# Optimization experiments

Measured on AMD Instinct MI355X. Metric: run time of the kernel, lower is better.

## Reference

```python
import jax, jax.numpy as jnp
import numpy as np

B, T, D = 2, 2048, 1024
HEADS, UNITS = 16, 64
OUT_DIM = 1024
_LARGE_BIAS = 10000.0


def _uniform(key, shape, fan_in, fan_out):
    limit = np.sqrt(6.0 / (fan_in + fan_out))
    return jax.random.uniform(key, shape, jnp.float32, -limit, limit)


def setup_inputs() -> dict:
    key = jax.random.key(0)
    kx, kq, kk, kv, ko = jax.random.split(key, 5)
    x = jax.random.normal(kx, (B, T, D), jnp.float32)
    mask = jnp.ones((B, T), jnp.int32)
    Wq = _uniform(kq, (D, HEADS * UNITS), D, UNITS)
    Wk = _uniform(kk, (D, HEADS * UNITS), D, UNITS)
    Wv = _uniform(kv, (D, HEADS * UNITS), D, UNITS)
    Wo = _uniform(ko, (HEADS * UNITS, OUT_DIM), HEADS * UNITS, OUT_DIM)
    return {"x": x, "mask": mask, "Wq": Wq, "Wk": Wk, "Wv": Wv, "Wo": Wo}


def reference(x, mask, Wq, Wk, Wv, Wo):
    m = mask.astype(x.dtype)                      # [B, T]
    x = x * m[:, :, None]                         # zero padded positions
    b, t, _ = x.shape
    # projections, split heads: [B, T, H, U]
    q = (x @ Wq).reshape(b, t, HEADS, UNITS)
    k = (x @ Wk).reshape(b, t, HEADS, UNITS)
    v = (x @ Wv).reshape(b, t, HEADS, UNITS)
    # logits[b,h,i,j] = sum_u q[b,i,h,u] k[b,j,h,u]
    logits = jnp.einsum('bihu,bjhu->bhij', q, k) / np.sqrt(UNITS).astype(x.dtype)
    # causal (forward) mask: subtract large bias above the diagonal
    causal = jnp.triu(jnp.full((t, t), _LARGE_BIAS, x.dtype), k=1)
    logits = logits - causal
    # padding mask on key axis
    logits = logits - ((1.0 - m) * _LARGE_BIAS)[:, None, None, :]
    weights = jax.nn.softmax(logits, axis=-1)     # [B, H, T, T]
    attended = jnp.einsum('bhij,bjhu->bihu', weights, v)
    attended = attended.reshape(b, t, HEADS * UNITS)
    return attended @ Wo                          # [B, T, OUT_DIM]
```

## Files before the change

kernel.cpp:

```cpp
#include <hip/hip_runtime.h>
#include <stdint.h>
#include <stddef.h>

#define B_ 2
#define T_ 2048
#define D_ 1024
#define H_ 16
#define U_ 64
#define M_ (B_ * T_)
#define N_ (H_ * U_)

typedef __attribute__((ext_vector_type(4))) float f32x4;
typedef __attribute__((ext_vector_type(8))) short s16x8;
typedef __attribute__((ext_vector_type(8))) __bf16 b16x8;

static_assert(sizeof(s16x8) == 16, "frag size");

__device__ __forceinline__ unsigned short f2bf(float f) {
  unsigned int u = __float_as_uint(f);
  u += 0x7FFFu + ((u >> 16) & 1u);
  return (unsigned short)(u >> 16);
}

__device__ __forceinline__ float exp2_hw(float x) {
  float r;
  asm("v_exp_f32 %0, %1" : "=v"(r) : "v"(x));
  return r;
}
__device__ __forceinline__ unsigned int cvtpk_bf16(float lo, float hi) {
  unsigned int r;
  asm("v_cvt_pk_bf16_f32 %0, %1, %2" : "=v"(r) : "v"(lo), "v"(hi));
  return r;
}

template <typename V>
__device__ __forceinline__ auto mfma16_impl(V a, V b, f32x4 c, int)
    -> decltype(__builtin_amdgcn_mfma_f32_16x16x32_bf16(a, b, c, 0, 0, 0)) {
  return __builtin_amdgcn_mfma_f32_16x16x32_bf16(a, b, c, 0, 0, 0);
}
template <typename V>
__device__ __forceinline__ f32x4 mfma16_impl(V a, V b, f32x4 c, long) {
  return __builtin_amdgcn_mfma_f32_16x16x32_bf16(
      __builtin_bit_cast(b16x8, a), __builtin_bit_cast(b16x8, b), c, 0, 0, 0);
}
__device__ __forceinline__ f32x4 mfma16(s16x8 a, s16x8 b, f32x4 c) {
  return mfma16_impl(a, b, c, 0);
}

__device__ __forceinline__ void gld16(const unsigned short* g, unsigned short* l) {
  __builtin_amdgcn_global_load_lds(
      (const __attribute__((address_space(1))) void*)g,
      (__attribute__((address_space(3))) void*)l, 16, 0, 0);
}

__global__ void wtrans_kernel(const float* __restrict__ w0, const float* __restrict__ w1,
                              const float* __restrict__ w2, const float* __restrict__ w3,
                              unsigned short* __restrict__ o0, unsigned short* __restrict__ o1,
                              unsigned short* __restrict__ o2, unsigned short* __restrict__ o3) {
  __shared__ float tile[64][65];
  const float* w;
  unsigned short* o;
  switch (blockIdx.z) {
    case 0: w = w0; o = o0; break;
    case 1: w = w1; o = o1; break;
    case 2: w = w2; o = o2; break;
    default: w = w3; o = o3; break;
  }
  const int kb = blockIdx.y * 64, nb = blockIdx.x * 64;
  const int tid = threadIdx.x;
  const int r0 = tid >> 6, c = tid & 63;
#pragma unroll
  for (int i = 0; i < 16; i++) {
    int r = i * 4 + r0;
    tile[r][c] = w[(size_t)(kb + r) * 1024 + nb + c];
  }
  __syncthreads();
#pragma unroll
  for (int i = 0; i < 16; i++) {
    int r = i * 4 + r0;
    o[(size_t)(nb + r) * 1024 + kb + c] = f2bf(tile[c][r]);
  }
}

__global__ void xmask_kernel(const float* __restrict__ x, const int* __restrict__ mask,
                             unsigned short* __restrict__ xb) {
  const int idx = (blockIdx.x * 256 + threadIdx.x) * 4;
  const int row = idx >> 10;
  const float m = (float)mask[row];
  float4 v = *(const float4*)(x + idx);
  ushort4 o;
  o.x = f2bf(v.x * m);
  o.y = f2bf(v.y * m);
  o.z = f2bf(v.z * m);
  o.w = f2bf(v.w * m);
  *(ushort4*)(xb + idx) = o;
}

template <int MODE>
__device__ __forceinline__ void gemm97_body(const unsigned short* __restrict__ A,
                                            const unsigned short* __restrict__ Bt,
                                            void* __restrict__ Cout) {
  constexpr int Kd = 1024, Nd = 1024;
  __shared__ unsigned short la[128 * 32];
  __shared__ unsigned short lb[128 * 32];
  const int tid = threadIdx.x;
  const int lane = tid & 63;
  const int w = tid >> 6;
  const int mb = blockIdx.y * 128, nb = blockIdx.x * 128;
  const int wm = (w >> 1) * 64, wn = (w & 1) * 64;
  const int lr = lane & 15, lg = lane >> 4;
  const int srow = w * 16 + (lane >> 2);
  const int scol = (lane & 3) * 8;
  const unsigned short* gA = A + (size_t)(mb + srow) * Kd + scol;
  const unsigned short* gB = Bt + (size_t)(nb + srow) * Kd + scol;
  unsigned short* lA = la + srow * 32 + scol;
  unsigned short* lB = lb + srow * 32 + scol;

  f32x4 acc[4][4] = {};

  for (int kt = 0; kt < Kd; kt += 32) {
    gld16(gA + kt, lA);
    gld16(gA + kt + (size_t)64 * Kd, lA + 64 * 32);
    gld16(gB + kt, lB);
    gld16(gB + kt + (size_t)64 * Kd, lB + 64 * 32);
    __syncthreads();
    s16x8 af[4], bfr[4];
#pragma unroll
    for (int i = 0; i < 4; i++)
      af[i] = *(const s16x8*)(la + (wm + i * 16 + lr) * 32 + lg * 8);
#pragma unroll
    for (int j = 0; j < 4; j++)
      bfr[j] = *(const s16x8*)(lb + (wn + j * 16 + lr) * 32 + lg * 8);
#pragma unroll
    for (int i = 0; i < 4; i++)
#pragma unroll
      for (int j = 0; j < 4; j++)
        acc[i][j] = mfma16(af[i], bfr[j], acc[i][j]);
    __syncthreads();
  }

#pragma unroll
  for (int i = 0; i < 4; i++)
#pragma unroll
    for (int j = 0; j < 4; j++) {
      const int col = nb + wn + j * 16 + lr;
      const int rowb = mb + wm + i * 16 + lg * 4;
      if (MODE == 1) {
        float* C = (float*)Cout;
#pragma unroll
        for (int r = 0; r < 4; r++) C[(size_t)(rowb + r) * Nd + col] = acc[i][j][r];
      } else if (MODE == 0) {
        unsigned short* C = (unsigned short*)Cout;
#pragma unroll
        for (int r = 0; r < 4; r++) C[(size_t)(rowb + r) * Nd + col] = f2bf(acc[i][j][r]);
      } else {
        unsigned short* C = (unsigned short*)Cout;
        const size_t vrow = ((size_t)(rowb >> 11) * 16 + (col >> 6)) * 64 + (col & 63);
        ushort4 o;
#pragma unroll
        for (int r = 0; r < 4; r++) ((unsigned short*)&o)[r] = f2bf(acc[i][j][r]);
        *(ushort4*)(C + vrow * T_ + (rowb & 2047)) = o;
      }
    }
}

__global__ __launch_bounds__(256) void gemm_qkv(const unsigned short* __restrict__ A,
                                                const unsigned short* __restrict__ wq,
                                                const unsigned short* __restrict__ wk,
                                                const unsigned short* __restrict__ wv,
                                                unsigned short* __restrict__ cq,
                                                unsigned short* __restrict__ ck,
                                                unsigned short* __restrict__ vt) {
  if (blockIdx.z == 0) {
    gemm97_body<0>(A, wq, cq);
  } else if (blockIdx.z == 1) {
    gemm97_body<0>(A, wk, ck);
  } else {
    gemm97_body<2>(A, wv, vt);
  }
}

__global__ __launch_bounds__(256) void gemm_out(const unsigned short* __restrict__ A,
                                                const unsigned short* __restrict__ woT,
                                                float* __restrict__ C) {
  gemm97_body<1>(A, woT, C);
}

__global__ __launch_bounds__(64) void attn17_kernel(const unsigned short* __restrict__ Q,
                                                    const unsigned short* __restrict__ K,
                                                    const unsigned short* __restrict__ Vt,
                                                    const int* __restrict__ mask,
                                                    unsigned short* __restrict__ att) {
  __shared__ unsigned short pbuf[32 * 64];
  const int lane = threadIdx.x & 63;
  const int li = lane & 15, lg = lane >> 4;
  const int bh = blockIdx.x & 31;
  const int b = bh >> 4, h = bh & 15;
  const int pr = blockIdx.x >> 5;

  const float CS = 0.125f * 1.44269504089f;
  const float PB = 10000.0f * 1.44269504089f;
  const float THR = 8.0f;

  const unsigned short* Kb = K + (size_t)(b * T_) * 1024 + h * 64;
  const unsigned short* Vtb = Vt + (size_t)bh * 64 * T_;
  const int* mk = mask + b * T_;

  const int xr = (li & 3) << 5;
  char* pbb = (char*)pbuf;

  for (int g = 0; g < 2; g++) {
    const int qg = g == 0 ? (63 - pr) : pr;
    const int q0 = qg * 32;

    s16x8 qf[2][2];
#pragma unroll
    for (int f = 0; f < 2; f++) {
      const unsigned short* qrow = Q + ((size_t)(b * T_) + q0 + f * 16 + li) * 1024 + h * 64;
      qf[f][0] = *(const s16x8*)(qrow + lg * 8);
      qf[f][1] = *(const s16x8*)(qrow + 32 + lg * 8);
    }

    const int iq0 = q0 + li, iq1 = q0 + 16 + li;

    float mrun[2] = {-1e30f, -1e30f};
    f32x4 lp[2] = {};
    f32x4 acc[4][2] = {};
    s16x8 vf[4][2];

    const int ntiles = (q0 + 95) >> 6;

    auto loadK = [&](s16x8 (&dst)[4][2], int jb) {
#pragma unroll
      for (int jf = 0; jf < 4; jf++) {
        const unsigned short* kr = Kb + (size_t)(jb + jf * 16 + li) * 1024 + lg * 8;
        dst[jf][0] = *(const s16x8*)kr;
        dst[jf][1] = *(const s16x8*)(kr + 32);
      }
    };
    auto loadM = [&](int4 (&dst)[4], int jb) {
#pragma unroll
      for (int jf = 0; jf < 4; jf++)
        dst[jf] = *(const int4*)(mk + jb + jf * 16 + lg * 4);
    };
    auto loadV = [&](int jb) {
#pragma unroll
      for (int uf = 0; uf < 4; uf++) {
        const unsigned short* vr = Vtb + (size_t)(uf * 16 + li) * T_ + jb + lg * 8;
        vf[uf][0] = *(const s16x8*)vr;
        vf[uf][1] = *(const s16x8*)(vr + 32);
      }
    };
    auto qk = [&](f32x4 (&s)[4][2], s16x8 (&kc)[4][2]) {
      __builtin_amdgcn_s_setprio(1);
#pragma unroll
      for (int jf = 0; jf < 4; jf++) {
        f32x4 z = {};
        s[jf][0] = mfma16(kc[jf][0], qf[0][0], z);
        s[jf][0] = mfma16(kc[jf][1], qf[0][1], s[jf][0]);
        f32x4 z2 = {};
        s[jf][1] = mfma16(kc[jf][0], qf[1][0], z2);
        s[jf][1] = mfma16(kc[jf][1], qf[1][1], s[jf][1]);
      }
      __builtin_amdgcn_s_setprio(0);
    };
    auto smw = [&](f32x4 (&s)[4][2], int4 (&mv)[4], int jb) {
      const bool diag = (jb + 64 > q0);
      const int band = (mv[0].x & mv[0].y & mv[0].z & mv[0].w) &
                       (mv[1].x & mv[1].y & mv[1].z & mv[1].w) &
                       (mv[2].x & mv[2].y & mv[2].z & mv[2].w) &
                       (mv[3].x & mv[3].y & mv[3].z & mv[3].w);
      const bool noBias = __all(band != 0);
#pragma unroll
      for (int f = 0; f < 2; f++) {
        const int iq = f ? iq1 : iq0;
        f32x4 pv4 = {-3e38f, -3e38f, -3e38f, -3e38f};
        if (noBias) {
#pragma unroll
          for (int jf = 0; jf < 4; jf++) {
            f32x4 zz = s[jf][f] * CS;
            if (diag) {
#pragma unroll
              for (int r = 0; r < 4; r++)
                if (jb + jf * 16 + lg * 4 + r > iq) zz[r] = -1e30f;
            }
            s[jf][f] = zz;
            pv4 = __builtin_elementwise_max(pv4, zz);
          }
        } else {
#pragma unroll
          for (int jf = 0; jf < 4; jf++) {
            f32x4 zz;
#pragma unroll
            for (int r = 0; r < 4; r++) {
              float z = fmaf(s[jf][f][r], CS, ((&mv[jf].x)[r] ? 0.f : -PB));
              if (diag && (jb + jf * 16 + lg * 4 + r > iq)) z = -1e30f;
              zz[r] = z;
            }
            s[jf][f] = zz;
            pv4 = __builtin_elementwise_max(pv4, zz);
          }
        }
        const float pmax = fmaxf(fmaxf(pv4[0], pv4[1]), fmaxf(pv4[2], pv4[3]));
        if (!__all(pmax <= mrun[f] + THR)) {
          float rmax = fmaxf(pmax, __shfl_xor(pmax, 16));
          rmax = fmaxf(rmax, __shfl_xor(rmax, 32));
          const float mnew = fmaxf(mrun[f], rmax);
          const float al = exp2_hw(mrun[f] - mnew);
          lp[f] *= al;
#pragma unroll
          for (int uf = 0; uf < 4; uf++) acc[uf][f] *= al;
          mrun[f] = mnew;
        }
        const float mm = mrun[f];
#pragma unroll
        for (int jf = 0; jf < 4; jf++) {
          f32x4 p;
#pragma unroll
          for (int r = 0; r < 4; r++) p[r] = exp2_hw(s[jf][f][r] - mm);
          lp[f] += p;
          uint2 w2;
          w2.x = cvtpk_bf16(p[0], p[1]);
          w2.y = cvtpk_bf16(p[2], p[3]);
          const int wb = (((f * 16 + li) * 64 + jf * 16 + lg * 4) * 2) ^ xr;
          *(uint2*)(pbb + wb) = w2;
        }
      }
    };
    auto pv = [&]() {
      s16x8 pfrag[2][2];
#pragma unroll
      for (int f = 0; f < 2; f++)
#pragma unroll
        for (int hh = 0; hh < 2; hh++) {
          const int rd = (((f * 16 + li) * 64 + hh * 32 + lg * 8) * 2) ^ xr;
          pfrag[f][hh] = *(const s16x8*)(pbb + rd);
        }
      __builtin_amdgcn_s_setprio(1);
#pragma unroll
      for (int uf = 0; uf < 4; uf++)
#pragma unroll
        for (int f = 0; f < 2; f++) {
          acc[uf][f] = mfma16(vf[uf][0], pfrag[f][0], acc[uf][f]);
          acc[uf][f] = mfma16(vf[uf][1], pfrag[f][1], acc[uf][f]);
        }
      __builtin_amdgcn_s_setprio(0);
    };

    s16x8 kA[4][2], kB[4][2];
    f32x4 sA[4][2], sB[4][2];
    int4 mA[4], mB[4];

    loadK(kA, 0);
    loadM(mA, 0);
    qk(sA, kA);
    if (ntiles > 1) {
      loadK(kB, 64);
      loadM(mB, 64);
    }

    int t = 0;
    while (true) {
      {
        const int jb = t * 64;
        loadV(jb);
        smw(sA, mA, jb);
        if (t + 1 < ntiles) qk(sB, kB);
        if (t + 2 < ntiles) {
          loadK(kA, (t + 2) * 64);
          loadM(mA, (t + 2) * 64);
        }
        pv();
      }
      if (t + 1 >= ntiles) break;
      {
        const int jb = (t + 1) * 64;
        loadV(jb);
        smw(sB, mB, jb);
        if (t + 2 < ntiles) qk(sA, kA);
        if (t + 3 < ntiles) {
          loadK(kB, (t + 3) * 64);
          loadM(mB, (t + 3) * 64);
        }
        pv();
      }
      t += 2;
      if (t >= ntiles) break;
    }

#pragma unroll
    for (int f = 0; f < 2; f++) {
      float l = (lp[f][0] + lp[f][1]) + (lp[f][2] + lp[f][3]);
      l += __shfl_xor(l, 16);
      l += __shfl_xor(l, 32);
      const float inv = 1.0f / l;
      unsigned short* arow = att + ((size_t)(b * T_) + q0 + f * 16 + li) * 1024 + h * 64;
#pragma unroll
      for (int uf = 0; uf < 4; uf++) {
        ushort4 o;
#pragma unroll
        for (int r = 0; r < 4; r++)
          ((unsigned short*)&o)[r] = __builtin_bit_cast(unsigned short, (__bf16)(acc[uf][f][r] * inv));
        *(ushort4*)(arow + uf * 16 + lg * 4) = o;
      }
    }
  }
}

extern "C" void kernel_launch(void* const* d_in, const int* in_sizes, int n_in,
                              void* d_out, int out_size, void* d_ws, size_t ws_size,
                              hipStream_t stream) {
  const float* x = (const float*)d_in[0];
  const int* mask = (const int*)d_in[1];
  const float* Wq = (const float*)d_in[2];
  const float* Wk = (const float*)d_in[3];
  const float* Wv = (const float*)d_in[4];
  const float* Wo = (const float*)d_in[5];

  const size_t MB = 1u << 20;
  char* ws = (char*)d_ws;
  unsigned short* wqT = (unsigned short*)(ws + 0 * MB);
  unsigned short* wkT = (unsigned short*)(ws + 2 * MB);
  unsigned short* wvT = (unsigned short*)(ws + 4 * MB);
  unsigned short* woT = (unsigned short*)(ws + 6 * MB);
  unsigned short* xb  = (unsigned short*)(ws + 8 * MB);
  unsigned short* qb  = (unsigned short*)(ws + 16 * MB);
  unsigned short* kb  = (unsigned short*)(ws + 24 * MB);
  unsigned short* vt  = (unsigned short*)(ws + 32 * MB);
  unsigned short* att = xb;
  (void)ws_size; (void)in_sizes; (void)n_in; (void)out_size;

  wtrans_kernel<<<dim3(16, 16, 4), 256, 0, stream>>>(Wq, Wk, Wv, Wo, wqT, wkT, wvT, woT);
  xmask_kernel<<<dim3(4096), 256, 0, stream>>>(x, mask, xb);
  gemm_qkv<<<dim3(8, 32, 3), 256, 0, stream>>>(xb, wqT, wkT, wvT, qb, kb, vt);
  attn17_kernel<<<dim3(1024), 64, 0, stream>>>(qb, kb, vt, mask, att);
  gemm_out<<<dim3(8, 32), 256, 0, stream>>>(att, woT, (float*)d_out);
}
```

Baseline: 141.1 us.

## Merge prep kernels and deepen GEMM K-tile to 64 with XOR-swizzled LDS

```diff
diff --git a/kernel.cpp b/kernel.cpp
--- a/kernel.cpp
+++ b/kernel.cpp
@@ -53,89 +53,99 @@
       (__attribute__((address_space(3))) void*)l, 16, 0, 0);
 }
 
-__global__ void wtrans_kernel(const float* __restrict__ w0, const float* __restrict__ w1,
-                              const float* __restrict__ w2, const float* __restrict__ w3,
-                              unsigned short* __restrict__ o0, unsigned short* __restrict__ o1,
-                              unsigned short* __restrict__ o2, unsigned short* __restrict__ o3) {
-  __shared__ float tile[64][65];
-  const float* w;
-  unsigned short* o;
-  switch (blockIdx.z) {
-    case 0: w = w0; o = o0; break;
-    case 1: w = w1; o = o1; break;
-    case 2: w = w2; o = o2; break;
-    default: w = w3; o = o3; break;
+__global__ void prep_kernel(const float* __restrict__ x, const int* __restrict__ mask,
+                            const float* __restrict__ w0, const float* __restrict__ w1,
+                            const float* __restrict__ w2, const float* __restrict__ w3,
+                            unsigned short* __restrict__ o0, unsigned short* __restrict__ o1,
+                            unsigned short* __restrict__ o2, unsigned short* __restrict__ o3,
+                            unsigned short* __restrict__ xb) {
+  const int tid = threadIdx.x;
+  if (blockIdx.x < 1024) {
+    __shared__ float tile[64][65];
+    const int id = blockIdx.x;
+    const int mz = id >> 8, by = (id >> 4) & 15, bx = id & 15;
+    const float* w;
+    unsigned short* o;
+    switch (mz) {
+      case 0: w = w0; o = o0; break;
+      case 1: w = w1; o = o1; break;
+      case 2: w = w2; o = o2; break;
+      default: w = w3; o = o3; break;
+    }
+    const int kb = by * 64, nb = bx * 64;
+    const int r0 = tid >> 6, c = tid & 63;
+#pragma unroll
+    for (int i = 0; i < 16; i++) {
+      int r = i * 4 + r0;
+      tile[r][c] = w[(size_t)(kb + r) * 1024 + nb + c];
+    }
+    __syncthreads();
+#pragma unroll
+    for (int i = 0; i < 16; i++) {
+      int r = i * 4 + r0;
+      o[(size_t)(nb + r) * 1024 + kb + c] = f2bf(tile[c][r]);
+    }
+  } else {
+    const int idx = ((blockIdx.x - 1024) * 256 + tid) * 4;
+    const int row = idx >> 10;
+    const float m = (float)mask[row];
+    float4 v = *(const float4*)(x + idx);
+    ushort4 o;
+    o.x = f2bf(v.x * m);
+    o.y = f2bf(v.y * m);
+    o.z = f2bf(v.z * m);
+    o.w = f2bf(v.w * m);
+    *(ushort4*)(xb + idx) = o;
   }
-  const int kb = blockIdx.y * 64, nb = blockIdx.x * 64;
-  const int tid = threadIdx.x;
-  const int r0 = tid >> 6, c = tid & 63;
-#pragma unroll
-  for (int i = 0; i < 16; i++) {
-    int r = i * 4 + r0;
-    tile[r][c] = w[(size_t)(kb + r) * 1024 + nb + c];
-  }
-  __syncthreads();
-#pragma unroll
-  for (int i = 0; i < 16; i++) {
-    int r = i * 4 + r0;
-    o[(size_t)(nb + r) * 1024 + kb + c] = f2bf(tile[c][r]);
-  }
-}
-
-__global__ void xmask_kernel(const float* __restrict__ x, const int* __restrict__ mask,
-                             unsigned short* __restrict__ xb) {
-  const int idx = (blockIdx.x * 256 + threadIdx.x) * 4;
-  const int row = idx >> 10;
-  const float m = (float)mask[row];
-  float4 v = *(const float4*)(x + idx);
-  ushort4 o;
-  o.x = f2bf(v.x * m);
-  o.y = f2bf(v.y * m);
-  o.z = f2bf(v.z * m);
-  o.w = f2bf(v.w * m);
-  *(ushort4*)(xb + idx) = o;
 }
 
 template <int MODE>
-__device__ __forceinline__ void gemm97_body(const unsigned short* __restrict__ A,
+__device__ __forceinline__ void gemm64_body(const unsigned short* __restrict__ A,
                                             const unsigned short* __restrict__ Bt,
                                             void* __restrict__ Cout) {
   constexpr int Kd = 1024, Nd = 1024;
-  __shared__ unsigned short la[128 * 32];
-  __shared__ unsigned short lb[128 * 32];
+  __shared__ unsigned short la[128 * 64];
+  __shared__ unsigned short lb[128 * 64];
   const int tid = threadIdx.x;
   const int lane = tid & 63;
   const int w = tid >> 6;
   const int mb = blockIdx.y * 128, nb = blockIdx.x * 128;
   const int wm = (w >> 1) * 64, wn = (w & 1) * 64;
   const int lr = lane & 15, lg = lane >> 4;
-  const int srow = w * 16 + (lane >> 2);
-  const int scol = (lane & 3) * 8;
-  const unsigned short* gA = A + (size_t)(mb + srow) * Kd + scol;
-  const unsigned short* gB = Bt + (size_t)(nb + srow) * Kd + scol;
-  unsigned short* lA = la + srow * 32 + scol;
-  unsigned short* lB = lb + srow * 32 + scol;
+  const int srow = tid >> 3;
+  const int scol = (tid & 7) * 8;
+  const int sc = scol ^ ((srow & 7) << 3);
+  const unsigned short* gA = A + (size_t)(mb + srow) * Kd + sc;
+  const unsigned short* gB = Bt + (size_t)(nb + srow) * Kd + sc;
+  unsigned short* lA = la + srow * 64 + scol;
+  unsigned short* lB = lb + srow * 64 + scol;
+  const int rsw = (lr & 7) << 3;
 
   f32x4 acc[4][4] = {};
 
-  for (int kt = 0; kt < Kd; kt += 32) {
-    gld16(gA + kt, lA);
-    gld16(gA + kt + (size_t)64 * Kd, lA + 64 * 32);
-    gld16(gB + kt, lB);
-    gld16(gB + kt + (size_t)64 * Kd, lB + 64 * 32);
+  for (int kt = 0; kt < Kd; kt += 64) {
+#pragma unroll
+    for (int i = 0; i < 4; i++) {
+      gld16(gA + kt + (size_t)(i * 32) * Kd, lA + i * 32 * 64);
+      gld16(gB + kt + (size_t)(i * 32) * Kd, lB + i * 32 * 64);
+    }
     __syncthreads();
-    s16x8 af[4], bfr[4];
-#pragma unroll
-    for (int i = 0; i < 4; i++)
-      af[i] = *(const s16x8*)(la + (wm + i * 16 + lr) * 32 + lg * 8);
-#pragma unroll
-    for (int j = 0; j < 4; j++)
-      bfr[j] = *(const s16x8*)(lb + (wn + j * 16 + lr) * 32 + lg * 8);
-#pragma unroll
-    for (int i = 0; i < 4; i++)
+#pragma unroll
+    for (int ks = 0; ks < 2; ks++) {
+      const int kc = (ks * 32 + lg * 8) ^ rsw;
+      s16x8 af[4], bfr[4];
+#pragma unroll
+      for (int i = 0; i < 4; i++)
+        af[i] = *(const s16x8*)(la + (wm + i * 16 + lr) * 64 + kc);
 #pragma unroll
       for (int j = 0; j < 4; j++)
-        acc[i][j] = mfma16(af[i], bfr[j], acc[i][j]);
+        bfr[j] = *(const s16x8*)(lb + (wn + j * 16 + lr) * 64 + kc);
+#pragma unroll
+      for (int i = 0; i < 4; i++)
+#pragma unroll
+        for (int j = 0; j < 4; j++)
+          acc[i][j] = mfma16(af[i], bfr[j], acc[i][j]);
+    }
     __syncthreads();
   }
 
@@ -172,18 +182,18 @@
                                                 unsigned short* __restrict__ ck,
                                                 unsigned short* __restrict__ vt) {
   if (blockIdx.z == 0) {
-    gemm97_body<0>(A, wq, cq);
+    gemm64_body<0>(A, wq, cq);
   } else if (blockIdx.z == 1) {
-    gemm97_body<0>(A, wk, ck);
+    gemm64_body<0>(A, wk, ck);
   } else {
-    gemm97_body<2>(A, wv, vt);
+    gemm64_body<2>(A, wv, vt);
   }
 }
 
 __global__ __launch_bounds__(256) void gemm_out(const unsigned short* __restrict__ A,
                                                 const unsigned short* __restrict__ woT,
                                                 float* __restrict__ C) {
-  gemm97_body<1>(A, woT, C);
+  gemm64_body<1>(A, woT, C);
 }
 
 __global__ __launch_bounds__(64) void attn17_kernel(const unsigned short* __restrict__ Q,
@@ -430,8 +440,8 @@
   unsigned short* att = xb;
   (void)ws_size; (void)in_sizes; (void)n_in; (void)out_size;
 
-  wtrans_kernel<<<dim3(16, 16, 4), 256, 0, stream>>>(Wq, Wk, Wv, Wo, wqT, wkT, wvT, woT);
-  xmask_kernel<<<dim3(4096), 256, 0, stream>>>(x, mask, xb);
+  prep_kernel<<<dim3(5120), 256, 0, stream>>>(x, mask, Wq, Wk, Wv, Wo,
+                                              wqT, wkT, wvT, woT, xb);
   gemm_qkv<<<dim3(8, 32, 3), 256, 0, stream>>>(xb, wqT, wkT, wvT, qb, kb, vt);
   attn17_kernel<<<dim3(1024), 64, 0, stream>>>(qb, kb, vt, mask, att);
   gemm_out<<<dim3(8, 32), 256, 0, stream>>>(att, woT, (float*)d_out);
```

Measured after the change: 140.9 us. Within noise of the previous version (-0.2%).
